# Optimization experiments

Measured on AMD Instinct MI355X. Metric: run time of the kernel, lower is better.

## Reference

```python
import jax, jax.numpy as jnp
import numpy as np

B, S, E, H = 4, 8192, 1024, 16
D = E // H  # head_dim = 64


def setup_inputs() -> dict:
    key = jax.random.key(0)
    ks = jax.random.split(key, 6)
    x = jax.random.normal(ks[0], (B, S, E), dtype=jnp.float32)
    key_padding_mask = jax.random.randint(ks[1], (B, S), 0, 2).astype(jnp.bool_)
    scale = 1.0 / np.sqrt(E)
    Wq = jax.random.normal(ks[2], (E, E), dtype=jnp.float32) * scale
    Wk = jax.random.normal(ks[3], (E, E), dtype=jnp.float32) * scale
    Wv = jax.random.normal(ks[4], (E, E), dtype=jnp.float32) * scale
    Wo = jax.random.normal(ks[5], (E, E), dtype=jnp.float32) * scale
    return {"x": x, "key_padding_mask": key_padding_mask,
            "Wq": Wq, "Wk": Wk, "Wv": Wv, "Wo": Wo}


def reference(x, key_padding_mask, Wq, Wk, Wv, Wo):
    b, s, _ = x.shape
    # torch Linear (no bias): y = x @ W.T
    Q = (x @ Wq.T).reshape(b, s, H, D).transpose(0, 2, 1, 3)  # (b,h,s,d)
    K = (x @ Wk.T).reshape(b, s, H, D).transpose(0, 2, 1, 3)
    V = (x @ Wv.T).reshape(b, s, H, D).transpose(0, 2, 1, 3)
    Q = jax.nn.elu(Q) + 1.0
    K = jax.nn.elu(K) + 1.0
    mask = key_padding_mask[:, None, :, None]  # (b,1,s,1), True = padding
    K = jnp.where(mask, 0.0, K)
    V = jnp.where(mask, 0.0, V)
    # global KV summarization over sequence: (b,h,d,e)
    KV = jnp.einsum('bhsd,bhse->bhde', K, V)
    K_sum = K.sum(axis=2)  # (b,h,d)
    Z = 1.0 / (jnp.einsum('bhsd,bhd->bhs', Q, K_sum) + 1e-6)  # (b,h,s)
    out = jnp.einsum('bhsd,bhde->bhse', Q, KV) * Z[..., None]  # (b,h,s,e)
    out = out.transpose(0, 2, 1, 3).reshape(b, s, E)
    return out @ Wo.T
```

## Files before the change

kernel.cpp:

```cpp
#include <hip/hip_runtime.h>

#define NB 4
#define NS 8192
#define NE 1024
#define NH 16
#define ND 64
#define NM (NB*NS)
#define NKT 16

typedef __bf16 bf16x8 __attribute__((ext_vector_type(8)));
typedef float  f32x4  __attribute__((ext_vector_type(4)));

__device__ __forceinline__ unsigned short f2bf(float f){
  unsigned int u = __float_as_uint(f);
  u += 0x7FFFu + ((u >> 16) & 1u);
  return (unsigned short)(u >> 16);
}
__device__ __forceinline__ float bf2f(unsigned short h){
  return __uint_as_float(((unsigned int)h) << 16);
}
__device__ __forceinline__ void gload16(const void* g, void* lds){
  __builtin_amdgcn_global_load_lds(
      (__attribute__((address_space(1))) unsigned int*)g,
      (__attribute__((address_space(3))) unsigned int*)lds, 16, 0, 0);
}

__global__ void mask_prep(const void* mraw, unsigned char* mask_u8){
  __shared__ int flag_s;
  if (threadIdx.x == 0) flag_s = 0;
  __syncthreads();
  const unsigned int* mi = (const unsigned int*)mraw;
  int bad = 0;
  for (int i = threadIdx.x; i < 4096; i += 256) bad |= (mi[i] > 1u) ? 1 : 0;
  if (bad) atomicOr(&flag_s, 1);
  __syncthreads();
  const int isbyte = flag_s;
  const unsigned char* mb = (const unsigned char*)mraw;
  int stride = gridDim.x * blockDim.x;
  for (int i = blockIdx.x*blockDim.x + threadIdx.x; i < NM; i += stride)
    mask_u8[i] = isbyte ? (unsigned char)(mb[i] != 0) : (unsigned char)(mi[i] != 0);
}

struct CastJobs {
  const float* src[5];
  unsigned short* dst[5];
  int n4[5];
};

__global__ __launch_bounds__(256) void castk(CastJobs J){
  int j = blockIdx.y;
  const float* s = J.src[j];
  unsigned short* d = J.dst[j];
  int n4 = J.n4[j];
  int stride = gridDim.x * blockDim.x;
  for (int i = blockIdx.x*blockDim.x + threadIdx.x; i < n4; i += stride){
    float4 v = *(const float4*)(s + (long)i*4);
    ushort4 o;
    o.x = f2bf(v.x); o.y = f2bf(v.y); o.z = f2bf(v.z); o.w = f2bf(v.w);
    *(ushort4*)(d + (long)i*4) = o;
  }
}

__global__ __launch_bounds__(512, 2) void gemm256(
    const unsigned short* __restrict__ A,
    const unsigned short* __restrict__ W0,
    const unsigned short* __restrict__ W1,
    const unsigned short* __restrict__ W2,
    unsigned short* __restrict__ O0,
    unsigned short* __restrict__ O1,
    unsigned short* __restrict__ O2,
    float* __restrict__ OF,
    const unsigned char* __restrict__ mask,
    int modeSel)
{
  __shared__ __align__(16) unsigned short As[2*256*64];
  __shared__ __align__(16) unsigned short Bs[2*256*64];

  const int mode = (modeSel < 0) ? (int)blockIdx.y : modeSel;
  const unsigned short* Bw = (mode==0) ? W0 : (mode==1) ? W1 : (mode==2) ? W2 : W0;
  unsigned short* Obf = (mode==0) ? O0 : (mode==1) ? O1 : O2;

  const int nwg = (int)gridDim.x;
  const int bx  = (int)blockIdx.x;
  const int swz = (bx & 7) * (nwg >> 3) + (bx >> 3);
  const long m0 = (long)(swz >> 2) * 256;
  const int  n0 = (swz & 3) * 256;

  const int tid = (int)threadIdx.x;
  const int l   = tid & 63;
  const int wv  = tid >> 6;
  const int wr  = wv >> 2;
  const int wc  = wv & 3;
  const int l15 = l & 15;
  const int lhi = l >> 4;
  const int swz8 = (l & 7) * 8;

  const int srow = wv*16 + (l >> 3);
  const int scol = ((l & 7) * 8) ^ ((l >> 3) << 3);

  auto stageA = [&](int st, int h){
    const long col = (long)st*64 + scol;
    #pragma unroll
    for (int is = 0; is < 2; ++is)
      gload16(A + (m0 + h*128 + srow + is*8)*NE + col,
              &As[(st & 1)*16384 + h*8192 + (wv*2 + is)*512]);
  };
  auto stageB = [&](int st, int h){
    const long col = (long)st*64 + scol;
    #pragma unroll
    for (int is = 0; is < 2; ++is)
      gload16(Bw + (long)(n0 + h*128 + srow + is*8)*NE + col,
              &Bs[(st & 1)*16384 + h*8192 + (wv*2 + is)*512]);
  };
  auto stageQ = [&](int s){
    if (s >= 4*NKT) return;
    const int st = s >> 2, qq = s & 3;
    if (qq & 2) stageB(st, qq & 1); else stageA(st, qq & 1);
  };

  auto lda = [&](int buf, int mi, int ks)->bf16x8 {
    const int row = wr*128 + mi*16 + l15;
    const int col = (ks*32 + lhi*8) ^ swz8;
    return *(const bf16x8*)&As[buf*16384 + row*64 + col];
  };
  auto ldb = [&](int buf, int ni, int ks)->bf16x8 {
    const int row = wc*64 + ni*16 + l15;
    const int col = (ks*32 + lhi*8) ^ swz8;
    return *(const bf16x8*)&Bs[buf*16384 + row*64 + col];
  };

  f32x4 acc[8][4];
  #pragma unroll
  for (int i=0;i<8;++i)
    #pragma unroll
    for (int j=0;j<4;++j)
      acc[i][j] = (f32x4){0.f,0.f,0.f,0.f};

  stageQ(0); stageQ(1); stageQ(2); stageQ(3);
  asm volatile("s_waitcnt vmcnt(4)" ::: "memory");
  stageQ(4); stageQ(5); stageQ(6);
  asm volatile("s_waitcnt vmcnt(6)" ::: "memory");
  __builtin_amdgcn_s_barrier();

  bf16x8 a0[4][2], a1[4][2], b0[2][2], b1[2][2];

  #pragma unroll 2
  for (int kt = 0; kt < NKT; ++kt){
    const int buf = kt & 1;
    const int sb  = 7 + 4*kt;

    #pragma unroll
    for (int i=0;i<4;++i){ a0[i][0]=lda(buf,i,0); a0[i][1]=lda(buf,i,1); }
    #pragma unroll
    for (int j=0;j<2;++j){ b0[j][0]=ldb(buf,j,0); b0[j][1]=ldb(buf,j,1); }
    stageQ(sb+0);
    asm volatile("s_waitcnt lgkmcnt(8)" ::: "memory");
    __builtin_amdgcn_s_barrier();
    asm volatile("s_waitcnt lgkmcnt(0)" ::: "memory");
    __builtin_amdgcn_sched_barrier(0);
    __builtin_amdgcn_s_setprio(1);
    #pragma unroll
    for (int ks=0;ks<2;++ks)
      #pragma unroll
      for (int i=0;i<4;++i)
        #pragma unroll
        for (int j=0;j<2;++j)
          acc[i][j] = __builtin_amdgcn_mfma_f32_16x16x32_bf16(a0[i][ks], b0[j][ks], acc[i][j], 0,0,0);
    __builtin_amdgcn_s_setprio(0);
    __builtin_amdgcn_s_barrier();

    #pragma unroll
    for (int i=0;i<4;++i){ a1[i][0]=lda(buf,4+i,0); a1[i][1]=lda(buf,4+i,1); }
    stageQ(sb+1);
    __builtin_amdgcn_s_barrier();
    asm volatile("s_waitcnt lgkmcnt(0)" ::: "memory");
    __builtin_amdgcn_sched_barrier(0);
    __builtin_amdgcn_s_setprio(1);
    #pragma unroll
    for (int ks=0;ks<2;++ks)
      #pragma unroll
      for (int i=0;i<4;++i)
        #pragma unroll
        for (int j=0;j<2;++j)
          acc[4+i][j] = __builtin_amdgcn_mfma_f32_16x16x32_bf16(a1[i][ks], b0[j][ks], acc[4+i][j], 0,0,0);
    __builtin_amdgcn_s_setprio(0);
    __builtin_amdgcn_s_barrier();

    #pragma unroll
    for (int j=0;j<2;++j){ b1[j][0]=ldb(buf,2+j,0); b1[j][1]=ldb(buf,2+j,1); }
    stageQ(sb+2);
    __builtin_amdgcn_s_barrier();
    asm volatile("s_waitcnt lgkmcnt(0)" ::: "memory");
    __builtin_amdgcn_sched_barrier(0);
    __builtin_amdgcn_s_setprio(1);
    #pragma unroll
    for (int ks=0;ks<2;++ks)
      #pragma unroll
      for (int i=0;i<4;++i)
        #pragma unroll
        for (int j=0;j<2;++j)
          acc[4+i][2+j] = __builtin_amdgcn_mfma_f32_16x16x32_bf16(a1[i][ks], b1[j][ks], acc[4+i][2+j], 0,0,0);
    __builtin_amdgcn_s_setprio(0);
    __builtin_amdgcn_s_barrier();

    stageQ(sb+3);
    __builtin_amdgcn_s_barrier();
    asm volatile("s_waitcnt lgkmcnt(0)" ::: "memory");
    __builtin_amdgcn_sched_barrier(0);
    __builtin_amdgcn_s_setprio(1);
    #pragma unroll
    for (int ks=0;ks<2;++ks)
      #pragma unroll
      for (int i=0;i<4;++i)
        #pragma unroll
        for (int j=0;j<2;++j)
          acc[i][2+j] = __builtin_amdgcn_mfma_f32_16x16x32_bf16(a0[i][ks], b1[j][ks], acc[i][2+j], 0,0,0);
    __builtin_amdgcn_s_setprio(0);
    if (kt < NKT-2)       asm volatile("s_waitcnt vmcnt(6)" ::: "memory");
    else if (kt == NKT-2) asm volatile("s_waitcnt vmcnt(0)" ::: "memory");
    __builtin_amdgcn_s_barrier();
  }

  #pragma unroll
  for (int mi=0;mi<8;++mi){
    #pragma unroll
    for (int r=0;r<4;++r){
      const long mg = m0 + wr*128 + mi*16 + lhi*4 + r;
      const bool mz = (mode==1 || mode==2) ? (mask[mg] != 0) : false;
      #pragma unroll
      for (int ni=0;ni<4;++ni){
        const int ng = n0 + wc*64 + ni*16 + l15;
        float v = acc[mi][ni][r];
        if (mode==0 || mode==1) v = (v > 0.f) ? (v + 1.f) : __expf(v);
        if (mz) v = 0.f;
        if (mode==3) OF[mg*NE + ng] = v;
        else         Obf[mg*NE + ng] = f2bf(v);
      }
    }
  }
}

#define KVCH 16
#define KVROWS (NS/KVCH)
__global__ __launch_bounds__(256) void kv_reduce(const unsigned short* __restrict__ K,
                                                 const unsigned short* __restrict__ V,
                                                 float* __restrict__ part){
  __shared__ float lds[2*64*68 + 192];
  float* Ksf = lds;
  float* Vsf = lds + 64*68;
  float* kcorner = lds + 2*64*68;

  const int bid = blockIdx.x;
  const int bh = bid >> 4;
  const int chunk = bid & 15;
  const int b = bh >> 4, h = bh & 15;
  const int t = threadIdx.x, w = t >> 6, l = t & 63;
  const int dg = l & 15, eg = l >> 4;
  const long base = ((long)b*NS + (long)chunk*KVROWS)*NE + h*ND;

  f32x4 acc[4][4];
  #pragma unroll
  for (int j=0;j<4;++j)
    #pragma unroll
    for (int q=0;q<4;++q)
      acc[j][q] = (f32x4){0.f,0.f,0.f,0.f};
  f32x4 ks4 = (f32x4){0.f,0.f,0.f,0.f};

  for (int sc = 0; sc < KVROWS/64; ++sc){
    if (sc) __syncthreads();
    const long rbase = base + (long)sc*64*NE;
    #pragma unroll
    for (int p = 0; p < 4; ++p){
      int g = p*256 + t;
      int row = g >> 4, col = (g & 15)*4;
      ushort4 ku = *(const ushort4*)(K + rbase + (long)row*NE + col);
      ushort4 vu = *(const ushort4*)(V + rbase + (long)row*NE + col);
      f32x4 kf = { bf2f(ku.x), bf2f(ku.y), bf2f(ku.z), bf2f(ku.w) };
      f32x4 vf = { bf2f(vu.x), bf2f(vu.y), bf2f(vu.z), bf2f(vu.w) };
      *(f32x4*)&Ksf[row*68 + col] = kf;
      *(f32x4*)&Vsf[row*68 + col] = vf;
    }
    __syncthreads();
    #pragma unroll 2
    for (int i = 0; i < 16; ++i){
      const int r = w*16 + i;
      f32x4 kq = *(const f32x4*)&Ksf[r*68 + dg*4];
      f32x4 v0 = *(const f32x4*)&Vsf[r*68 + eg*16 + 0];
      f32x4 v1 = *(const f32x4*)&Vsf[r*68 + eg*16 + 4];
      f32x4 v2 = *(const f32x4*)&Vsf[r*68 + eg*16 + 8];
      f32x4 v3 = *(const f32x4*)&Vsf[r*68 + eg*16 + 12];
      #pragma unroll
      for (int j=0;j<4;++j){
        const float kd = kq[j];
        acc[j][0] += kd * v0;
        acc[j][1] += kd * v1;
        acc[j][2] += kd * v2;
        acc[j][3] += kd * v3;
      }
      if (eg == 0) ks4 += kq;
    }
  }

  __syncthreads();
  if (w >= 1 && eg == 0)
    *(f32x4*)&kcorner[(w-1)*64 + dg*4] = ks4;
  if (w >= 2){
    float* reg = (w==2) ? Ksf : Vsf;
    #pragma unroll
    for (int j=0;j<4;++j)
      #pragma unroll
      for (int q=0;q<4;++q)
        *(f32x4*)&reg[l*68 + (j*4+q)*4] = acc[j][q];
  }
  __syncthreads();
  if (w < 2){
    float* reg = (w==0) ? Ksf : Vsf;
    #pragma unroll
    for (int j=0;j<4;++j)
      #pragma unroll
      for (int q=0;q<4;++q)
        acc[j][q] += *(const f32x4*)&reg[l*68 + (j*4+q)*4];
  }
  __syncthreads();
  if (w == 1){
    #pragma unroll
    for (int j=0;j<4;++j)
      #pragma unroll
      for (int q=0;q<4;++q)
        *(f32x4*)&Ksf[l*68 + (j*4+q)*4] = acc[j][q];
  }
  __syncthreads();
  if (w == 0){
    #pragma unroll
    for (int j=0;j<4;++j)
      #pragma unroll
      for (int q=0;q<4;++q)
        acc[j][q] += *(const f32x4*)&Ksf[l*68 + (j*4+q)*4];
    float* po = part + (long)(bh*16 + chunk)*4160;
    #pragma unroll
    for (int j=0;j<4;++j)
      #pragma unroll
      for (int q=0;q<4;++q)
        *(f32x4*)&po[(dg*4 + j)*64 + eg*16 + q*4] = acc[j][q];
    if (eg == 0){
      #pragma unroll
      for (int i=0;i<3;++i)
        ks4 += *(const f32x4*)&kcorner[i*64 + dg*4];
      *(f32x4*)&po[4096 + dg*4] = ks4;
    }
  }
}

__global__ __launch_bounds__(256) void kv_finish(const float* __restrict__ part,
                                                 unsigned short* __restrict__ KVfrag){
  __shared__ float KVf[64*65 + 32];
  const int bh = blockIdx.x, t = threadIdx.x;
  const float* pb = part + (long)bh*16*4160;

  #pragma unroll
  for (int p = 0; p < 4; ++p){
    int g = p*256 + t;
    f32x4 s = (f32x4){0.f,0.f,0.f,0.f};
    for (int c = 0; c < 16; ++c) s += *(const f32x4*)&pb[c*4160 + g*4];
    int d = g >> 4, e = (g & 15)*4;
    KVf[d*65 + e+0] = s[0];
    KVf[d*65 + e+1] = s[1];
    KVf[d*65 + e+2] = s[2];
    KVf[d*65 + e+3] = s[3];
  }
  if (t < 16){
    f32x4 s = (f32x4){0.f,0.f,0.f,0.f};
    for (int c = 0; c < 16; ++c) s += *(const f32x4*)&pb[c*4160 + 4096 + t*4];
    #pragma unroll
    for (int j=0;j<4;++j) KVf[(t*4+j)*65 + 64] = s[j];
  }
  __syncthreads();

  for (int idx = t; idx < 10240; idx += 256){
    int j   = idx & 7;
    int lfr = (idx >> 3) & 63;
    int grp = idx >> 9;
    int nt  = grp % 5, ks = grp / 5;
    int kk  = (ks & 1)*32 + (lfr >> 4)*8 + j;
    int n   = nt*16 + (lfr & 15);
    float v = (n <= 64) ? KVf[kk*65 + n] : 0.f;
    unsigned short hi = f2bf(v);
    unsigned short o  = (ks >> 1) ? f2bf(v - bf2f(hi)) : hi;
    KVfrag[(long)bh*10240 + idx] = o;
  }
}

__global__ __launch_bounds__(256) void attn_mfma(const unsigned short* __restrict__ Q,
                                                 const unsigned short* __restrict__ KVfrag,
                                                 unsigned short* __restrict__ attn){
  __shared__ unsigned short Qs[256*64];
  const int bid = blockIdx.x;
  const int bh = bid >> 5, chunk = bid & 31;
  const int b = bh >> 4, h = bh & 15;
  const int t = threadIdx.x, w = t >> 6, l = t & 63;
  const int l15 = l & 15, lhi = l >> 4;
  const long row0 = (long)b*NS + chunk*256;

  const int srccol = ((l & 7) ^ (l >> 3)) * 8;
  #pragma unroll
  for (int c = 0; c < 8; ++c){
    const int r = w*64 + c*8 + (l >> 3);
    gload16(Q + (row0 + r)*NE + h*ND + srccol, &Qs[(w*8 + c)*512]);
  }

  bf16x8 bf[4][5];
  #pragma unroll
  for (int ks=0; ks<4; ++ks)
    #pragma unroll
    for (int nt=0; nt<5; ++nt)
      bf[ks][nt] = *(const bf16x8*)(KVfrag + (long)bh*10240 + (ks*5+nt)*512 + l*8);

  __syncthreads();

  const int swz = (l15 & 7) << 4;
  const char* qbase = (const char*)&Qs[w*4096];

  #pragma unroll
  for (int rt=0; rt<4; ++rt){
    const int rb = (rt*16 + l15)*128;
    bf16x8 a0 = *(const bf16x8*)(qbase + rb + ((lhi*16) ^ swz));
    bf16x8 a1 = *(const bf16x8*)(qbase + rb + ((64 + lhi*16) ^ swz));
    f32x4 acc[5];
    #pragma unroll
    for (int nt=0; nt<5; ++nt){
      acc[nt] = (f32x4){0.f,0.f,0.f,0.f};
      acc[nt] = __builtin_amdgcn_mfma_f32_16x16x32_bf16(a0, bf[0][nt], acc[nt], 0,0,0);
      acc[nt] = __builtin_amdgcn_mfma_f32_16x16x32_bf16(a1, bf[1][nt], acc[nt], 0,0,0);
      acc[nt] = __builtin_amdgcn_mfma_f32_16x16x32_bf16(a0, bf[2][nt], acc[nt], 0,0,0);
      acc[nt] = __builtin_amdgcn_mfma_f32_16x16x32_bf16(a1, bf[3][nt], acc[nt], 0,0,0);
    }
    float dv[4];
    #pragma unroll
    for (int e=0;e<4;++e){
      float d = __shfl(acc[4][e], l & 48, 64);
      dv[e] = 1.f / (d + 1e-6f);
    }
    #pragma unroll
    for (int nt=0; nt<4; ++nt){
      #pragma unroll
      for (int e=0;e<4;++e){
        const int row = rt*16 + lhi*4 + e;
        const int cb  = (nt*16 + l15)*2;
        Qs[w*4096 + ((row*128 + (cb ^ ((row & 7) << 4))) >> 1)] = f2bf(acc[nt][e] * dv[e]);
      }
    }
  }

  asm volatile("s_waitcnt lgkmcnt(0)" ::: "memory");
  #pragma unroll
  for (int c=0;c<8;++c){
    const int r = c*8 + (l >> 3);
    bf16x8 vv = *(const bf16x8*)((const char*)&Qs[w*4096] + r*128 + ((((l&7) ^ (l>>3))) << 4));
    *(bf16x8*)(attn + (row0 + w*64 + r)*NE + h*ND + (l&7)*8) = vv;
  }
}

extern "C" void kernel_launch(void* const* d_in, const int* in_sizes, int n_in,
                              void* d_out, int out_size, void* d_ws, size_t ws_size,
                              hipStream_t stream){
  (void)in_sizes; (void)n_in; (void)out_size; (void)ws_size;
  const float* x    = (const float*)d_in[0];
  const void*  mraw = d_in[1];
  const float* Wq   = (const float*)d_in[2];
  const float* Wk   = (const float*)d_in[3];
  const float* Wv   = (const float*)d_in[4];
  const float* Wo   = (const float*)d_in[5];
  float* out = (float*)d_out;
  char* ws = (char*)d_ws;

  unsigned short* xb  = (unsigned short*)(ws + 0L);
  unsigned short* Wqb = (unsigned short*)(ws + 67108864L);
  unsigned short* Wkb = (unsigned short*)(ws + 69206016L);
  unsigned short* Wvb = (unsigned short*)(ws + 71303168L);
  unsigned short* Wob = (unsigned short*)(ws + 73400320L);
  unsigned short* Qb  = (unsigned short*)(ws + 75497472L);
  unsigned short* Kb  = (unsigned short*)(ws + 142606336L);
  unsigned short* Vb  = (unsigned short*)(ws + 209715200L);
  unsigned short* KVfrag = (unsigned short*)(ws + 276824064L);
  unsigned char* mask_u8 = (unsigned char*)(ws + 278462464L);
  float* part = (float*)xb;

  mask_prep<<<32, 256, 0, stream>>>(mraw, mask_u8);

  CastJobs J;
  J.src[0]=x;  J.dst[0]=xb;  J.n4[0]=NM*NE/4;
  J.src[1]=Wq; J.dst[1]=Wqb; J.n4[1]=NE*NE/4;
  J.src[2]=Wk; J.dst[2]=Wkb; J.n4[2]=NE*NE/4;
  J.src[3]=Wv; J.dst[3]=Wvb; J.n4[3]=NE*NE/4;
  J.src[4]=Wo; J.dst[4]=Wob; J.n4[4]=NE*NE/4;
  castk<<<dim3(1024,5), 256, 0, stream>>>(J);

  gemm256<<<dim3(512,3), 512, 0, stream>>>(xb, Wqb, Wkb, Wvb,
                                           Qb, Kb, Vb, nullptr, mask_u8, -1);

  kv_reduce<<<dim3(1024), 256, 0, stream>>>(Kb, Vb, part);
  kv_finish<<<dim3(64), 256, 0, stream>>>(part, KVfrag);

  attn_mfma<<<dim3(2048), 256, 0, stream>>>(Qb, KVfrag, xb);

  gemm256<<<dim3(512,1), 512, 0, stream>>>(xb, Wob, Wob, Wob,
                                           nullptr, nullptr, nullptr, out, mask_u8, 3);
}
```

Measured before the change: 476.8 us.

## Switch projection GEMM from 16x16x32 to 32x32x16 MFMA tiles

Replaces the 16x16x32 bf16 MFMA instructions in the projection GEMM with 32x32x16 MFMAs. The per-wave 128x64 output is now held in eight 32x32 accumulators. LDS fragment loads, the k-step split across the four phases, the lgkmcnt waits and the epilogue index mapping are all rewritten to match. The aim is fewer MFMA issues and fewer LDS reads per FLOP, through better operand reuse. The cost is a different register layout, and the epilogue stores become more scattered.

```diff
diff --git a/kernel.cpp b/kernel.cpp
--- a/kernel.cpp
+++ b/kernel.cpp
@@ -10,6 +10,7 @@
 
 typedef __bf16 bf16x8 __attribute__((ext_vector_type(8)));
 typedef float  f32x4  __attribute__((ext_vector_type(4)));
+typedef float  f32x16 __attribute__((ext_vector_type(16)));
 
 __device__ __forceinline__ unsigned short f2bf(float f){
   unsigned int u = __float_as_uint(f);
@@ -91,8 +92,8 @@
   const int wv  = tid >> 6;
   const int wr  = wv >> 2;
   const int wc  = wv & 3;
-  const int l15 = l & 15;
-  const int lhi = l >> 4;
+  const int l31 = l & 31;
+  const int lk  = l >> 5;
   const int swz8 = (l & 7) * 8;
 
   const int srow = wv*16 + (l >> 3);
@@ -119,22 +120,22 @@
   };
 
   auto lda = [&](int buf, int mi, int ks)->bf16x8 {
-    const int row = wr*128 + mi*16 + l15;
-    const int col = (ks*32 + lhi*8) ^ swz8;
+    const int row = wr*128 + mi*32 + l31;
+    const int col = (ks*16 + lk*8) ^ swz8;
     return *(const bf16x8*)&As[buf*16384 + row*64 + col];
   };
-  auto ldb = [&](int buf, int ni, int ks)->bf16x8 {
-    const int row = wc*64 + ni*16 + l15;
-    const int col = (ks*32 + lhi*8) ^ swz8;
+  auto ldb = [&](int buf, int nj, int ks)->bf16x8 {
+    const int row = wc*64 + nj*32 + l31;
+    const int col = (ks*16 + lk*8) ^ swz8;
     return *(const bf16x8*)&Bs[buf*16384 + row*64 + col];
   };
 
-  f32x4 acc[8][4];
-  #pragma unroll
-  for (int i=0;i<8;++i)
-    #pragma unroll
-    for (int j=0;j<4;++j)
-      acc[i][j] = (f32x4){0.f,0.f,0.f,0.f};
+  f32x16 acc[4][2];
+  #pragma unroll
+  for (int i=0;i<4;++i)
+    #pragma unroll
+    for (int j=0;j<2;++j)
+      acc[i][j] = (f32x16){0.f,0.f,0.f,0.f,0.f,0.f,0.f,0.f,0.f,0.f,0.f,0.f,0.f,0.f,0.f,0.f};
 
   stageQ(0); stageQ(1); stageQ(2); stageQ(3);
   asm volatile("s_waitcnt vmcnt(4)" ::: "memory");
@@ -142,7 +143,8 @@
   asm volatile("s_waitcnt vmcnt(6)" ::: "memory");
   __builtin_amdgcn_s_barrier();
 
-  bf16x8 a0[4][2], a1[4][2], b0[2][2], b1[2][2];
+  bf16x8 aa[4][4];
+  bf16x8 bn0[4], bn1[4];
 
   #pragma unroll 2
   for (int kt = 0; kt < NKT; ++kt){
@@ -150,11 +152,10 @@
     const int sb  = 7 + 4*kt;
 
     #pragma unroll
-    for (int i=0;i<4;++i){ a0[i][0]=lda(buf,i,0); a0[i][1]=lda(buf,i,1); }
-    #pragma unroll
-    for (int j=0;j<2;++j){ b0[j][0]=ldb(buf,j,0); b0[j][1]=ldb(buf,j,1); }
+    for (int i=0;i<4;++i){ aa[i][0]=lda(buf,i,0); aa[i][1]=lda(buf,i,1); }
+    bn0[0]=ldb(buf,0,0); bn0[1]=ldb(buf,0,1);
     stageQ(sb+0);
-    asm volatile("s_waitcnt lgkmcnt(8)" ::: "memory");
+    asm volatile("s_waitcnt lgkmcnt(6)" ::: "memory");
     __builtin_amdgcn_s_barrier();
     asm volatile("s_waitcnt lgkmcnt(0)" ::: "memory");
     __builtin_amdgcn_sched_barrier(0);
@@ -163,31 +164,28 @@
     for (int ks=0;ks<2;++ks)
       #pragma unroll
       for (int i=0;i<4;++i)
-        #pragma unroll
-        for (int j=0;j<2;++j)
-          acc[i][j] = __builtin_amdgcn_mfma_f32_16x16x32_bf16(a0[i][ks], b0[j][ks], acc[i][j], 0,0,0);
+        acc[i][0] = __builtin_amdgcn_mfma_f32_32x32x16_bf16(aa[i][ks], bn0[ks], acc[i][0], 0,0,0);
     __builtin_amdgcn_s_setprio(0);
     __builtin_amdgcn_s_barrier();
 
     #pragma unroll
-    for (int i=0;i<4;++i){ a1[i][0]=lda(buf,4+i,0); a1[i][1]=lda(buf,4+i,1); }
+    for (int i=0;i<4;++i){ aa[i][2]=lda(buf,i,2); aa[i][3]=lda(buf,i,3); }
+    bn0[2]=ldb(buf,0,2); bn0[3]=ldb(buf,0,3);
     stageQ(sb+1);
+    asm volatile("s_waitcnt lgkmcnt(6)" ::: "memory");
     __builtin_amdgcn_s_barrier();
     asm volatile("s_waitcnt lgkmcnt(0)" ::: "memory");
     __builtin_amdgcn_sched_barrier(0);
     __builtin_amdgcn_s_setprio(1);
     #pragma unroll
-    for (int ks=0;ks<2;++ks)
+    for (int ks=2;ks<4;++ks)
       #pragma unroll
       for (int i=0;i<4;++i)
-        #pragma unroll
-        for (int j=0;j<2;++j)
-          acc[4+i][j] = __builtin_amdgcn_mfma_f32_16x16x32_bf16(a1[i][ks], b0[j][ks], acc[4+i][j], 0,0,0);
+        acc[i][0] = __builtin_amdgcn_mfma_f32_32x32x16_bf16(aa[i][ks], bn0[ks], acc[i][0], 0,0,0);
     __builtin_amdgcn_s_setprio(0);
     __builtin_amdgcn_s_barrier();
 
-    #pragma unroll
-    for (int j=0;j<2;++j){ b1[j][0]=ldb(buf,2+j,0); b1[j][1]=ldb(buf,2+j,1); }
+    bn1[0]=ldb(buf,1,0); bn1[1]=ldb(buf,1,1); bn1[2]=ldb(buf,1,2); bn1[3]=ldb(buf,1,3);
     stageQ(sb+2);
     __builtin_amdgcn_s_barrier();
     asm volatile("s_waitcnt lgkmcnt(0)" ::: "memory");
@@ -197,9 +195,7 @@
     for (int ks=0;ks<2;++ks)
       #pragma unroll
       for (int i=0;i<4;++i)
-        #pragma unroll
-        for (int j=0;j<2;++j)
-          acc[4+i][2+j] = __builtin_amdgcn_mfma_f32_16x16x32_bf16(a1[i][ks], b1[j][ks], acc[4+i][2+j], 0,0,0);
+        acc[i][1] = __builtin_amdgcn_mfma_f32_32x32x16_bf16(aa[i][ks], bn1[ks], acc[i][1], 0,0,0);
     __builtin_amdgcn_s_setprio(0);
     __builtin_amdgcn_s_barrier();
 
@@ -209,12 +205,10 @@
     __builtin_amdgcn_sched_barrier(0);
     __builtin_amdgcn_s_setprio(1);
     #pragma unroll
-    for (int ks=0;ks<2;++ks)
+    for (int ks=2;ks<4;++ks)
       #pragma unroll
       for (int i=0;i<4;++i)
-        #pragma unroll
-        for (int j=0;j<2;++j)
-          acc[i][2+j] = __builtin_amdgcn_mfma_f32_16x16x32_bf16(a0[i][ks], b1[j][ks], acc[i][2+j], 0,0,0);
+        acc[i][1] = __builtin_amdgcn_mfma_f32_32x32x16_bf16(aa[i][ks], bn1[ks], acc[i][1], 0,0,0);
     __builtin_amdgcn_s_setprio(0);
     if (kt < NKT-2)       asm volatile("s_waitcnt vmcnt(6)" ::: "memory");
     else if (kt == NKT-2) asm volatile("s_waitcnt vmcnt(0)" ::: "memory");
@@ -222,19 +216,22 @@
   }
 
   #pragma unroll
-  for (int mi=0;mi<8;++mi){
-    #pragma unroll
-    for (int r=0;r<4;++r){
-      const long mg = m0 + wr*128 + mi*16 + lhi*4 + r;
-      const bool mz = (mode==1 || mode==2) ? (mask[mg] != 0) : false;
-      #pragma unroll
-      for (int ni=0;ni<4;++ni){
-        const int ng = n0 + wc*64 + ni*16 + l15;
-        float v = acc[mi][ni][r];
-        if (mode==0 || mode==1) v = (v > 0.f) ? (v + 1.f) : __expf(v);
-        if (mz) v = 0.f;
-        if (mode==3) OF[mg*NE + ng] = v;
-        else         Obf[mg*NE + ng] = f2bf(v);
+  for (int mi=0;mi<4;++mi){
+    #pragma unroll
+    for (int oct=0; oct<4; ++oct){
+      #pragma unroll
+      for (int rr=0; rr<4; ++rr){
+        const long mg = m0 + wr*128 + mi*32 + oct*8 + lk*4 + rr;
+        const bool mz = (mode==1 || mode==2) ? (mask[mg] != 0) : false;
+        #pragma unroll
+        for (int nj=0; nj<2; ++nj){
+          const int ng = n0 + wc*64 + nj*32 + l31;
+          float v = acc[mi][nj][oct*4 + rr];
+          if (mode==0 || mode==1) v = (v > 0.f) ? (v + 1.f) : __expf(v);
+          if (mz) v = 0.f;
+          if (mode==3) OF[mg*NE + ng] = v;
+          else         Obf[mg*NE + ng] = f2bf(v);
+        }
       }
     }
   }
```

After: 520.9 us. +9.2%, slower.
